# Kernel optimization log

Measured on AMD Instinct MI355X. Metric: run time of the kernel, lower is better.

The kernel has to match this reference:

```python
import jax, jax.numpy as jnp
import numpy as np

NUM_VARIABLES = 20
NUM_LAYERS = 3
NUM_CONSTRAINTS = 64
NUM_STATES = 2 ** NUM_VARIABLES
TOP_K = 10  # min(10, num_states)


def _state_bits():
    # bits[i, v] = v-th bit of i, MSB first (matches format(i, '0{n}b'))
    idx = jnp.arange(NUM_STATES, dtype=jnp.int32)
    shifts = jnp.arange(NUM_VARIABLES - 1, -1, -1, dtype=jnp.int32)
    return ((idx[:, None] >> shifts[None, :]) & 1).astype(jnp.float32)


def setup_inputs() -> dict:
    key = jax.random.key(0)
    k1, k2, k3 = jax.random.split(key, 3)
    return {
        "problem_constraints": jax.random.normal(k1, (NUM_CONSTRAINTS, NUM_VARIABLES), dtype=jnp.float32),
        "beta_params": jax.random.normal(k2, (NUM_LAYERS,), dtype=jnp.float32) * 0.1,
        "gamma_params": jax.random.normal(k3, (NUM_LAYERS,), dtype=jnp.float32) * 0.1,
    }


def reference(problem_constraints, beta_params, gamma_params):
    bits = _state_bits()  # [S, n]
    # cost_function evaluated on every basis state (vectorized over 2^n states)
    viol = bits @ problem_constraints.T  # [S, C]
    costs = jnp.sum(jnp.maximum(viol - 1.0, 0.0) ** 2, axis=1) + 0.1 * jnp.sum(bits, axis=1)
    costs = jax.lax.stop_gradient(costs)  # torch fills costs via .item(), detaching them

    amps = jnp.full((NUM_STATES,), 1.0 / np.sqrt(NUM_STATES), dtype=jnp.float32)
    for layer in range(NUM_LAYERS):
        # problem unitary: exp(-i*gamma*cost) applied to real amps, then cast back
        # to float32 (torch .to(float) keeps the real part) => multiply by cos.
        amps = amps * jnp.cos(gamma_params[layer] * costs)
        # mixer: mixed[i] = amps[i] + 0.1*sin(beta) * sum_bit amps[i ^ (1<<bit)]
        grid = amps.reshape((2,) * NUM_VARIABLES)
        nb = jnp.zeros_like(grid)
        for ax in range(NUM_VARIABLES):  # structural loop over qubit axes
            nb = nb + jnp.flip(grid, axis=ax)
        mixed = amps + 0.1 * jnp.sin(beta_params[layer]) * nb.reshape(-1)
        amps = mixed / jnp.linalg.norm(mixed)

    probs = amps ** 2  # |amplitude|^2 (amps are real after the casts)
    _, top_idx = jax.lax.top_k(probs, TOP_K)
    top_assignments = bits[top_idx]  # [K, n]
    assignment_costs = costs[top_idx]  # same formula as cost_function on each
    best = jnp.argmin(assignment_costs)
    optimal_assignment = top_assignments[best]
    optimal_cost = assignment_costs[best]
    return (optimal_assignment, optimal_cost, probs, top_assignments, assignment_costs)
```

## Files before the change

kernel.cpp:

```cpp
#include <hip/hip_runtime.h>
#include <math.h>

#define NV 20
#define NC 64
#define NSTATES (1u << 20)
#define TOPK 10
#define NB1 256
#define NCAND (NB1 * TOPK)

__global__ __launch_bounds__(256) void k_costs(const float* __restrict__ C,
                                               float* __restrict__ costs,
                                               float* __restrict__ ph0,
                                               const float* __restrict__ gamma,
                                               double* __restrict__ scal,
                                               unsigned* __restrict__ ctr) {
    __shared__ float CT[NV][NC];
    __shared__ float lowT[8][NC];
    const int tid = threadIdx.x;

    if (blockIdx.x == 0) {
        if (tid < 8) scal[tid] = 0.0;
        if (tid == 8) *ctr = 0u;
    }

    for (int e = tid; e < NC * NV; e += 256) {
        int c = e / NV, j = e % NV;
        CT[j][c] = C[e];
    }
    for (int e = tid; e < 8 * NC; e += 256) {
        int m = e >> 6, c = e & 63;
        float v = 0.0f;
        if (m & 1) v += C[c * NV + 19];
        if (m & 2) v += C[c * NV + 18];
        if (m & 4) v += C[c * NV + 17];
        lowT[m][c] = v;
    }
    __syncthreads();

    unsigned t = blockIdx.x * 256u + (unsigned)tid;
    float g0 = gamma[0];

    float4 b[16];
    #pragma unroll
    for (int q = 0; q < 16; ++q) b[q] = make_float4(-1.f, -1.f, -1.f, -1.f);
    #pragma unroll
    for (int k = 0; k < 17; ++k) {
        float bf = (float)((t >> k) & 1u);
        const float4* row = (const float4*)(&CT[16 - k][0]);
        #pragma unroll
        for (int q = 0; q < 16; ++q) {
            float4 cv = row[q];
            b[q].x = fmaf(bf, cv.x, b[q].x);
            b[q].y = fmaf(bf, cv.y, b[q].y);
            b[q].z = fmaf(bf, cv.z, b[q].z);
            b[q].w = fmaf(bf, cv.w, b[q].w);
        }
    }

    float res[8], ph[8];
    #pragma unroll
    for (int s = 0; s < 8; ++s) {
        unsigned i = t * 8u + (unsigned)s;
        float cost = 0.1f * (float)__popc(i);
        const float4* lrow = (const float4*)(&lowT[s][0]);
        #pragma unroll
        for (int q = 0; q < 16; ++q) {
            float4 lv = lrow[q];
            float4 v;
            v.x = b[q].x + lv.x; v.y = b[q].y + lv.y;
            v.z = b[q].z + lv.z; v.w = b[q].w + lv.w;
            float r;
            r = fmaxf(v.x, 0.f); cost = fmaf(r, r, cost);
            r = fmaxf(v.y, 0.f); cost = fmaf(r, r, cost);
            r = fmaxf(v.z, 0.f); cost = fmaf(r, r, cost);
            r = fmaxf(v.w, 0.f); cost = fmaf(r, r, cost);
        }
        res[s] = cost;
        ph[s] = 0x1p-10f * cosf(g0 * cost);
    }
    float4* co = (float4*)(costs + (size_t)t * 8u);
    co[0] = make_float4(res[0], res[1], res[2], res[3]);
    co[1] = make_float4(res[4], res[5], res[6], res[7]);
    float4* po = (float4*)(ph0 + (size_t)t * 8u);
    po[0] = make_float4(ph[0], ph[1], ph[2], ph[3]);
    po[1] = make_float4(ph[4], ph[5], ph[6], ph[7]);
}

template <int LAYER, bool ALIN, bool ALOUT>
__global__ __launch_bounds__(1024, 4) void k_mix(const float* __restrict__ pin,
                                                 const float* __restrict__ costs,
                                                 float* __restrict__ pout,
                                                 const float* __restrict__ gamma,
                                                 const float* __restrict__ beta,
                                                 double* __restrict__ scal) {
    __shared__ float4 tile[1024];
    __shared__ double dpart[16];
    const unsigned lq = threadIdx.x;
    const unsigned i4 = blockIdx.x * 1024u + lq;
    float s = 0.1f * sinf(beta[LAYER]);
    float prevscale = (LAYER == 0) ? 1.0f : (float)(1.0 / sqrt(scal[LAYER - 1]));

    auto ld4 = [&](unsigned j4) -> float4 {
        if (ALIN) return ((const float4*)pin)[j4];
        float4 a;
        a.x = pin[4u * j4 + 0]; a.y = pin[4u * j4 + 1];
        a.z = pin[4u * j4 + 2]; a.w = pin[4u * j4 + 3];
        return a;
    };

    float4 own = ld4(i4);
    tile[lq] = own;

    float4 gv[8];
    #pragma unroll
    for (int p = 19; p >= 12; --p) gv[19 - p] = ld4(i4 ^ (1u << (p - 2)));

    __syncthreads();

    float4 nb = make_float4(0.f, 0.f, 0.f, 0.f);
    #pragma unroll
    for (int u = 0; u < 8; ++u) {
        nb.x += gv[u].x; nb.y += gv[u].y; nb.z += gv[u].z; nb.w += gv[u].w;
    }
    #pragma unroll
    for (int p = 11; p >= 2; --p) {
        float4 v = tile[lq ^ (1u << (p - 2))];
        nb.x += v.x; nb.y += v.y; nb.z += v.z; nb.w += v.w;
    }
    nb.x += own.z; nb.y += own.w; nb.z += own.x; nb.w += own.y;
    nb.x += own.y; nb.y += own.x; nb.z += own.w; nb.w += own.z;

    float4 m;
    m.x = prevscale * fmaf(s, nb.x, own.x);
    m.y = prevscale * fmaf(s, nb.y, own.y);
    m.z = prevscale * fmaf(s, nb.z, own.z);
    m.w = prevscale * fmaf(s, nb.w, own.w);

    float4 o;
    if (LAYER < 2) {
        float gn = gamma[LAYER + 1];
        float4 c = ((const float4*)costs)[i4];
        o.x = m.x * cosf(gn * c.x);
        o.y = m.y * cosf(gn * c.y);
        o.z = m.z * cosf(gn * c.z);
        o.w = m.w * cosf(gn * c.w);
    } else {
        o = m;
    }
    if (ALOUT) {
        ((float4*)pout)[i4] = o;
    } else {
        pout[4u * i4 + 0] = o.x; pout[4u * i4 + 1] = o.y;
        pout[4u * i4 + 2] = o.z; pout[4u * i4 + 3] = o.w;
    }

    double ss = (double)m.x * m.x + (double)m.y * m.y +
                (double)m.z * m.z + (double)m.w * m.w;
    #pragma unroll
    for (int off = 32; off > 0; off >>= 1) ss += __shfl_down(ss, off);
    int wid = threadIdx.x >> 6;
    if ((threadIdx.x & 63) == 0) dpart[wid] = ss;
    __syncthreads();
    if (threadIdx.x == 0) {
        double t = 0.0;
        #pragma unroll
        for (int w = 0; w < 16; ++w) t += dpart[w];
        atomicAdd(&scal[LAYER], t);
    }
}

template <bool ALIN>
__global__ __launch_bounds__(256) void k_ptop(const float* __restrict__ A,
                                              const double* __restrict__ scal2,
                                              const float* __restrict__ costs,
                                              float* __restrict__ out,
                                              unsigned long long* __restrict__ cand,
                                              unsigned* __restrict__ ctr) {
    __shared__ unsigned long long warr[4];
    __shared__ int lastblk;
    __shared__ unsigned topi[TOPK];
    __shared__ float topc[TOPK];
    const int tid = threadIdx.x;
    float* probs_out = out + 21;
    unsigned b4 = blockIdx.x * 1024u;
    float scale = (float)(1.0 / sqrt(*scal2));

    unsigned long long k[16];
    #pragma unroll
    for (int u = 0; u < 4; ++u) {
        unsigned j4 = b4 + (unsigned)tid + 256u * u;
        float4 v;
        if (ALIN) v = ((const float4*)A)[j4];
        else {
            v.x = A[4u * j4 + 0]; v.y = A[4u * j4 + 1];
            v.z = A[4u * j4 + 2]; v.w = A[4u * j4 + 3];
        }
        float4 p;
        p.x = v.x * scale; p.x *= p.x;
        p.y = v.y * scale; p.y *= p.y;
        p.z = v.z * scale; p.z *= p.z;
        p.w = v.w * scale; p.w *= p.w;
        unsigned e0 = 4u * j4;
        probs_out[e0 + 0] = p.x; probs_out[e0 + 1] = p.y;
        probs_out[e0 + 2] = p.z; probs_out[e0 + 3] = p.w;
        k[4 * u + 0] = ((unsigned long long)__float_as_uint(p.x) << 32) | (unsigned long long)(0xFFFFFFFFu - (e0 + 0));
        k[4 * u + 1] = ((unsigned long long)__float_as_uint(p.y) << 32) | (unsigned long long)(0xFFFFFFFFu - (e0 + 1));
        k[4 * u + 2] = ((unsigned long long)__float_as_uint(p.z) << 32) | (unsigned long long)(0xFFFFFFFFu - (e0 + 2));
        k[4 * u + 3] = ((unsigned long long)__float_as_uint(p.w) << 32) | (unsigned long long)(0xFFFFFFFFu - (e0 + 3));
    }

    for (int r = 0; r < TOPK; ++r) {
        unsigned long long loc = 0ull;
        #pragma unroll
        for (int j = 0; j < 16; ++j) if (k[j] > loc) loc = k[j];
        #pragma unroll
        for (int off = 32; off > 0; off >>= 1) {
            unsigned long long o = __shfl_down(loc, off);
            if (o > loc) loc = o;
        }
        if ((tid & 63) == 0) warr[tid >> 6] = loc;
        __syncthreads();
        unsigned long long win = warr[0];
        if (warr[1] > win) win = warr[1];
        if (warr[2] > win) win = warr[2];
        if (warr[3] > win) win = warr[3];
        __syncthreads();
        #pragma unroll
        for (int j = 0; j < 16; ++j) if (k[j] == win) k[j] = 0ull;
        if (tid == 0) cand[blockIdx.x * TOPK + r] = win;
    }

    __threadfence();
    if (tid == 0) {
        unsigned old = atomicAdd(ctr, 1u);
        lastblk = (old == NB1 - 1) ? 1 : 0;
    }
    __syncthreads();
    if (!lastblk) return;
    __threadfence();

    unsigned long long c2[TOPK];
    #pragma unroll
    for (int u = 0; u < TOPK; ++u) c2[u] = cand[tid + 256 * u];

    for (int r = 0; r < TOPK; ++r) {
        unsigned long long loc = 0ull;
        #pragma unroll
        for (int u = 0; u < TOPK; ++u) if (c2[u] > loc) loc = c2[u];
        #pragma unroll
        for (int off = 32; off > 0; off >>= 1) {
            unsigned long long o = __shfl_down(loc, off);
            if (o > loc) loc = o;
        }
        if ((tid & 63) == 0) warr[tid >> 6] = loc;
        __syncthreads();
        unsigned long long win = warr[0];
        if (warr[1] > win) win = warr[1];
        if (warr[2] > win) win = warr[2];
        if (warr[3] > win) win = warr[3];
        __syncthreads();
        #pragma unroll
        for (int u = 0; u < TOPK; ++u) if (c2[u] == win) c2[u] = 0ull;
        if (tid == 0) topi[r] = 0xFFFFFFFFu - (unsigned)(win & 0xFFFFFFFFull);
        __syncthreads();
    }

    const unsigned S = NSTATES;
    if (tid < TOPK * NV) {
        int kk = tid / NV, vv = tid % NV;
        out[21 + S + (unsigned)tid] = (float)((topi[kk] >> (NV - 1 - vv)) & 1u);
    }
    if (tid < TOPK) {
        float c = costs[topi[tid]];
        topc[tid] = c;
        out[21 + S + TOPK * NV + (unsigned)tid] = c;
    }
    __syncthreads();
    if (tid == 0) {
        int best = 0;
        for (int kk = 1; kk < TOPK; ++kk)
            if (topc[kk] < topc[best]) best = kk;
        unsigned gi = topi[best];
        for (int vv = 0; vv < NV; ++vv)
            out[vv] = (float)((gi >> (NV - 1 - vv)) & 1u);
        out[NV] = topc[best];
    }
}

extern "C" void kernel_launch(void* const* d_in, const int* in_sizes, int n_in,
                              void* d_out_, int out_size, void* d_ws, size_t ws_size,
                              hipStream_t stream) {
    (void)in_sizes; (void)n_in; (void)out_size;
    const float* C     = (const float*)d_in[0];
    const float* beta  = (const float*)d_in[1];
    const float* gamma = (const float*)d_in[2];
    float* out = (float*)d_out_;
    char* ws = (char*)d_ws;
    const size_t S4 = (size_t)NSTATES * sizeof(float);

    double* scal = (double*)ws;
    unsigned* ctr = (unsigned*)(ws + 64);
    unsigned long long* cand = (unsigned long long*)(ws + 1024);
    float* costs = (float*)(ws + 32768);
    float* A     = (float*)(ws + 32768 + S4);
    const size_t need_full = 32768 + 3 * S4;
    bool wsbig = (ws_size >= need_full);
    float* B = wsbig ? (float*)(ws + 32768 + 2 * S4) : (out + 21);

    k_costs<<<512, 256, 0, stream>>>(C, costs, A, gamma, scal, ctr);

    if (wsbig) {
        k_mix<0, true, true ><<<256, 1024, 0, stream>>>(A, costs, B, gamma, beta, scal);
        k_mix<1, true, true ><<<256, 1024, 0, stream>>>(B, costs, A, gamma, beta, scal);
        k_mix<2, true, true ><<<256, 1024, 0, stream>>>(A, costs, B, gamma, beta, scal);
        k_ptop<true ><<<NB1, 256, 0, stream>>>(B, scal + 2, costs, out, cand, ctr);
    } else {
        k_mix<0, true, false><<<256, 1024, 0, stream>>>(A, costs, B, gamma, beta, scal);
        k_mix<1, false, true><<<256, 1024, 0, stream>>>(B, costs, A, gamma, beta, scal);
        k_mix<2, true, false><<<256, 1024, 0, stream>>>(A, costs, B, gamma, beta, scal);
        k_ptop<false><<<NB1, 256, 0, stream>>>(B, scal + 2, costs, out, cand, ctr);
    }
}
```

Before: 89.55 us.

## Fuse cost, mixer layers and top-k into one cooperative persistent kernel

```diff
diff --git a/kernel.cpp b/kernel.cpp
--- a/kernel.cpp
+++ b/kernel.cpp
@@ -1,12 +1,284 @@
 #include <hip/hip_runtime.h>
+#include <hip/hip_cooperative_groups.h>
 #include <math.h>
+
+namespace cg = cooperative_groups;
 
 #define NV 20
 #define NC 64
 #define NSTATES (1u << 20)
 #define TOPK 10
-#define NB1 256
-#define NCAND (NB1 * TOPK)
+#define NBLK 256
+#define NTHR 1024
+#define NCAND (NBLK * TOPK)
+#define NB1F 256
+
+template <bool ALB>
+__global__ __launch_bounds__(NTHR, 4) void k_all(
+    const float* __restrict__ C,
+    const float* __restrict__ beta,
+    const float* __restrict__ gamma,
+    float* __restrict__ costs,
+    float* __restrict__ A,
+    float* __restrict__ B,
+    float* __restrict__ out,
+    double* __restrict__ scal,
+    unsigned long long* __restrict__ cand) {
+
+  cg::grid_group grid = cg::this_grid();
+
+  __shared__ float4 tile[NTHR];
+  __shared__ float CT[17][NC];
+  __shared__ float lowT[8][NC];
+  __shared__ double dpart[16];
+  __shared__ unsigned long long warr[16];
+  __shared__ unsigned long long winS;
+  __shared__ unsigned topi[TOPK];
+  __shared__ float topc[TOPK];
+
+  const int tid = threadIdx.x;
+  const unsigned t = blockIdx.x * (unsigned)NTHR + (unsigned)tid;
+
+  if (blockIdx.x == 0 && tid < 8) scal[tid] = 0.0;
+
+  for (int e = tid; e < 17 * NC; e += NTHR) {
+    int k = e / NC, c = e % NC;
+    CT[k][c] = C[c * NV + (16 - k)];
+  }
+  for (int e = tid; e < 8 * NC; e += NTHR) {
+    int m = e >> 6, c = e & 63;
+    float v = 0.0f;
+    if (m & 1) v += C[c * NV + 19];
+    if (m & 2) v += C[c * NV + 18];
+    if (m & 4) v += C[c * NV + 17];
+    lowT[m][c] = v;
+  }
+  __syncthreads();
+
+  float4 b[16];
+  #pragma unroll
+  for (int q = 0; q < 16; ++q) b[q] = make_float4(-1.f, -1.f, -1.f, -1.f);
+  #pragma unroll
+  for (int k = 0; k < 17; ++k) {
+    float bf = (float)((t >> (k + 1)) & 1u);
+    const float4* row = (const float4*)(&CT[k][0]);
+    #pragma unroll
+    for (int q = 0; q < 16; ++q) {
+      float4 cv = row[q];
+      b[q].x = fmaf(bf, cv.x, b[q].x);
+      b[q].y = fmaf(bf, cv.y, b[q].y);
+      b[q].z = fmaf(bf, cv.z, b[q].z);
+      b[q].w = fmaf(bf, cv.w, b[q].w);
+    }
+  }
+
+  float g0 = gamma[0];
+  float c_own[4], p_arr[4];
+  #pragma unroll
+  for (int s = 0; s < 4; ++s) {
+    unsigned i = 4u * t + (unsigned)s;
+    float cost = 0.1f * (float)__popc(i);
+    int m = (int)(((t & 1u) << 2) | (unsigned)s);
+    const float4* lrow = (const float4*)(&lowT[m][0]);
+    #pragma unroll
+    for (int q = 0; q < 16; ++q) {
+      float4 lv = lrow[q];
+      float4 v;
+      v.x = b[q].x + lv.x; v.y = b[q].y + lv.y;
+      v.z = b[q].z + lv.z; v.w = b[q].w + lv.w;
+      float r;
+      r = fmaxf(v.x, 0.f); cost = fmaf(r, r, cost);
+      r = fmaxf(v.y, 0.f); cost = fmaf(r, r, cost);
+      r = fmaxf(v.z, 0.f); cost = fmaf(r, r, cost);
+      r = fmaxf(v.w, 0.f); cost = fmaf(r, r, cost);
+    }
+    c_own[s] = cost;
+    p_arr[s] = 0x1p-10f * cosf(g0 * cost);
+  }
+  ((float4*)costs)[t] = make_float4(c_own[0], c_own[1], c_own[2], c_own[3]);
+  float4 pin_own = make_float4(p_arr[0], p_arr[1], p_arr[2], p_arr[3]);
+  ((float4*)A)[t] = pin_own;
+
+  grid.sync();
+
+  float4 m2_own = make_float4(0.f, 0.f, 0.f, 0.f);
+  #pragma unroll
+  for (int L = 0; L < 3; ++L) {
+    const float* pin = (L == 1) ? B : A;
+    const bool pinAligned = (L == 1) ? ALB : true;
+    float s = 0.1f * sinf(beta[L]);
+    float prevscale = (L == 0) ? 1.0f : (float)(1.0 / sqrt(scal[L - 1]));
+
+    tile[tid] = pin_own;
+    float4 gv[8];
+    #pragma unroll
+    for (int p = 19; p >= 12; --p) {
+      unsigned j4 = t ^ (1u << (p - 2));
+      if (pinAligned) gv[19 - p] = ((const float4*)pin)[j4];
+      else {
+        gv[19 - p].x = pin[4u * j4 + 0]; gv[19 - p].y = pin[4u * j4 + 1];
+        gv[19 - p].z = pin[4u * j4 + 2]; gv[19 - p].w = pin[4u * j4 + 3];
+      }
+    }
+    __syncthreads();
+
+    float4 nb = make_float4(0.f, 0.f, 0.f, 0.f);
+    #pragma unroll
+    for (int u = 0; u < 8; ++u) {
+      nb.x += gv[u].x; nb.y += gv[u].y; nb.z += gv[u].z; nb.w += gv[u].w;
+    }
+    #pragma unroll
+    for (int p = 11; p >= 2; --p) {
+      float4 v = tile[tid ^ (1 << (p - 2))];
+      nb.x += v.x; nb.y += v.y; nb.z += v.z; nb.w += v.w;
+    }
+    nb.x += pin_own.z; nb.y += pin_own.w; nb.z += pin_own.x; nb.w += pin_own.y;
+    nb.x += pin_own.y; nb.y += pin_own.x; nb.z += pin_own.w; nb.w += pin_own.z;
+
+    float4 m;
+    m.x = prevscale * fmaf(s, nb.x, pin_own.x);
+    m.y = prevscale * fmaf(s, nb.y, pin_own.y);
+    m.z = prevscale * fmaf(s, nb.z, pin_own.z);
+    m.w = prevscale * fmaf(s, nb.w, pin_own.w);
+
+    double ss = (double)m.x * m.x + (double)m.y * m.y +
+                (double)m.z * m.z + (double)m.w * m.w;
+    #pragma unroll
+    for (int off = 32; off > 0; off >>= 1) ss += __shfl_down(ss, off);
+    if ((tid & 63) == 0) dpart[tid >> 6] = ss;
+    __syncthreads();
+    if (tid == 0) {
+      double tt = 0.0;
+      #pragma unroll
+      for (int w = 0; w < 16; ++w) tt += dpart[w];
+      atomicAdd(&scal[L], tt);
+    }
+
+    if (L < 2) {
+      float gn = gamma[L + 1];
+      float4 o;
+      o.x = m.x * cosf(gn * c_own[0]);
+      o.y = m.y * cosf(gn * c_own[1]);
+      o.z = m.z * cosf(gn * c_own[2]);
+      o.w = m.w * cosf(gn * c_own[3]);
+      if (L == 0) {
+        if (ALB) ((float4*)B)[t] = o;
+        else {
+          B[4u * t + 0] = o.x; B[4u * t + 1] = o.y;
+          B[4u * t + 2] = o.z; B[4u * t + 3] = o.w;
+        }
+      } else {
+        ((float4*)A)[t] = o;
+      }
+      pin_own = o;
+    } else {
+      m2_own = m;
+    }
+    grid.sync();
+  }
+
+  float scale2 = (float)(1.0 / sqrt(scal[2]));
+  float4 pr;
+  pr.x = m2_own.x * scale2; pr.x *= pr.x;
+  pr.y = m2_own.y * scale2; pr.y *= pr.y;
+  pr.z = m2_own.z * scale2; pr.z *= pr.z;
+  pr.w = m2_own.w * scale2; pr.w *= pr.w;
+  float* probs = out + 21;
+  unsigned e0 = 4u * t;
+  probs[e0 + 0] = pr.x; probs[e0 + 1] = pr.y;
+  probs[e0 + 2] = pr.z; probs[e0 + 3] = pr.w;
+
+  unsigned long long k[4];
+  k[0] = ((unsigned long long)__float_as_uint(pr.x) << 32) | (unsigned long long)(0xFFFFFFFFu - (e0 + 0));
+  k[1] = ((unsigned long long)__float_as_uint(pr.y) << 32) | (unsigned long long)(0xFFFFFFFFu - (e0 + 1));
+  k[2] = ((unsigned long long)__float_as_uint(pr.z) << 32) | (unsigned long long)(0xFFFFFFFFu - (e0 + 2));
+  k[3] = ((unsigned long long)__float_as_uint(pr.w) << 32) | (unsigned long long)(0xFFFFFFFFu - (e0 + 3));
+
+  for (int r = 0; r < TOPK; ++r) {
+    unsigned long long loc = k[0];
+    if (k[1] > loc) loc = k[1];
+    if (k[2] > loc) loc = k[2];
+    if (k[3] > loc) loc = k[3];
+    #pragma unroll
+    for (int off = 32; off > 0; off >>= 1) {
+      unsigned long long o = __shfl_down(loc, off);
+      if (o > loc) loc = o;
+    }
+    if ((tid & 63) == 0) warr[tid >> 6] = loc;
+    __syncthreads();
+    if (tid == 0) {
+      unsigned long long win = warr[0];
+      #pragma unroll
+      for (int w = 1; w < 16; ++w) if (warr[w] > win) win = warr[w];
+      winS = win;
+      cand[blockIdx.x * TOPK + r] = win;
+    }
+    __syncthreads();
+    unsigned long long win = winS;
+    if (k[0] == win) k[0] = 0ull;
+    if (k[1] == win) k[1] = 0ull;
+    if (k[2] == win) k[2] = 0ull;
+    if (k[3] == win) k[3] = 0ull;
+    __syncthreads();
+  }
+
+  grid.sync();
+
+  if (blockIdx.x != 0) return;
+
+  unsigned long long c2[3] = {0ull, 0ull, 0ull};
+  #pragma unroll
+  for (int u = 0; u < 3; ++u) {
+    int j = tid + NTHR * u;
+    if (j < NCAND) c2[u] = cand[j];
+  }
+  for (int r = 0; r < TOPK; ++r) {
+    unsigned long long loc = c2[0];
+    if (c2[1] > loc) loc = c2[1];
+    if (c2[2] > loc) loc = c2[2];
+    #pragma unroll
+    for (int off = 32; off > 0; off >>= 1) {
+      unsigned long long o = __shfl_down(loc, off);
+      if (o > loc) loc = o;
+    }
+    if ((tid & 63) == 0) warr[tid >> 6] = loc;
+    __syncthreads();
+    if (tid == 0) {
+      unsigned long long win = warr[0];
+      #pragma unroll
+      for (int w = 1; w < 16; ++w) if (warr[w] > win) win = warr[w];
+      winS = win;
+      topi[r] = 0xFFFFFFFFu - (unsigned)(win & 0xFFFFFFFFull);
+    }
+    __syncthreads();
+    unsigned long long win = winS;
+    if (c2[0] == win) c2[0] = 0ull;
+    if (c2[1] == win) c2[1] = 0ull;
+    if (c2[2] == win) c2[2] = 0ull;
+    __syncthreads();
+  }
+
+  const unsigned S = NSTATES;
+  if (tid < TOPK * NV) {
+    int kk = tid / NV, vv = tid % NV;
+    out[21 + S + (unsigned)tid] = (float)((topi[kk] >> (NV - 1 - vv)) & 1u);
+  }
+  if (tid < TOPK) {
+    float c = costs[topi[tid]];
+    topc[tid] = c;
+    out[21 + S + TOPK * NV + (unsigned)tid] = c;
+  }
+  __syncthreads();
+  if (tid == 0) {
+    int best = 0;
+    for (int kk = 1; kk < TOPK; ++kk)
+      if (topc[kk] < topc[best]) best = kk;
+    unsigned gi = topi[best];
+    for (int vv = 0; vv < NV; ++vv)
+      out[vv] = (float)((gi >> (NV - 1 - vv)) & 1u);
+    out[NV] = topc[best];
+  }
+}
 
 __global__ __launch_bounds__(256) void k_costs(const float* __restrict__ C,
                                                float* __restrict__ costs,
@@ -17,16 +289,11 @@
     __shared__ float CT[NV][NC];
     __shared__ float lowT[8][NC];
     const int tid = threadIdx.x;
-
     if (blockIdx.x == 0) {
         if (tid < 8) scal[tid] = 0.0;
         if (tid == 8) *ctr = 0u;
     }
-
-    for (int e = tid; e < NC * NV; e += 256) {
-        int c = e / NV, j = e % NV;
-        CT[j][c] = C[e];
-    }
+    for (int e = tid; e < NC * NV; e += 256) { int c = e / NV, j = e % NV; CT[j][c] = C[e]; }
     for (int e = tid; e < 8 * NC; e += 256) {
         int m = e >> 6, c = e & 63;
         float v = 0.0f;
@@ -36,10 +303,8 @@
         lowT[m][c] = v;
     }
     __syncthreads();
-
     unsigned t = blockIdx.x * 256u + (unsigned)tid;
     float g0 = gamma[0];
-
     float4 b[16];
     #pragma unroll
     for (int q = 0; q < 16; ++q) b[q] = make_float4(-1.f, -1.f, -1.f, -1.f);
@@ -56,7 +321,6 @@
             b[q].w = fmaf(bf, cv.w, b[q].w);
         }
     }
-
     float res[8], ph[8];
     #pragma unroll
     for (int s = 0; s < 8; ++s) {
@@ -99,7 +363,6 @@
     const unsigned i4 = blockIdx.x * 1024u + lq;
     float s = 0.1f * sinf(beta[LAYER]);
     float prevscale = (LAYER == 0) ? 1.0f : (float)(1.0 / sqrt(scal[LAYER - 1]));
-
     auto ld4 = [&](unsigned j4) -> float4 {
         if (ALIN) return ((const float4*)pin)[j4];
         float4 a;
@@ -107,21 +370,15 @@
         a.z = pin[4u * j4 + 2]; a.w = pin[4u * j4 + 3];
         return a;
     };
-
     float4 own = ld4(i4);
     tile[lq] = own;
-
     float4 gv[8];
     #pragma unroll
     for (int p = 19; p >= 12; --p) gv[19 - p] = ld4(i4 ^ (1u << (p - 2)));
-
-    __syncthreads();
-
+    __syncthreads();
     float4 nb = make_float4(0.f, 0.f, 0.f, 0.f);
     #pragma unroll
-    for (int u = 0; u < 8; ++u) {
-        nb.x += gv[u].x; nb.y += gv[u].y; nb.z += gv[u].z; nb.w += gv[u].w;
-    }
+    for (int u = 0; u < 8; ++u) { nb.x += gv[u].x; nb.y += gv[u].y; nb.z += gv[u].z; nb.w += gv[u].w; }
     #pragma unroll
     for (int p = 11; p >= 2; --p) {
         float4 v = tile[lq ^ (1u << (p - 2))];
@@ -129,43 +386,34 @@
     }
     nb.x += own.z; nb.y += own.w; nb.z += own.x; nb.w += own.y;
     nb.x += own.y; nb.y += own.x; nb.z += own.w; nb.w += own.z;
-
     float4 m;
     m.x = prevscale * fmaf(s, nb.x, own.x);
     m.y = prevscale * fmaf(s, nb.y, own.y);
     m.z = prevscale * fmaf(s, nb.z, own.z);
     m.w = prevscale * fmaf(s, nb.w, own.w);
-
     float4 o;
     if (LAYER < 2) {
         float gn = gamma[LAYER + 1];
         float4 c = ((const float4*)costs)[i4];
-        o.x = m.x * cosf(gn * c.x);
-        o.y = m.y * cosf(gn * c.y);
-        o.z = m.z * cosf(gn * c.z);
-        o.w = m.w * cosf(gn * c.w);
-    } else {
-        o = m;
-    }
-    if (ALOUT) {
-        ((float4*)pout)[i4] = o;
-    } else {
+        o.x = m.x * cosf(gn * c.x); o.y = m.y * cosf(gn * c.y);
+        o.z = m.z * cosf(gn * c.z); o.w = m.w * cosf(gn * c.w);
+    } else o = m;
+    if (ALOUT) ((float4*)pout)[i4] = o;
+    else {
         pout[4u * i4 + 0] = o.x; pout[4u * i4 + 1] = o.y;
         pout[4u * i4 + 2] = o.z; pout[4u * i4 + 3] = o.w;
     }
-
-    double ss = (double)m.x * m.x + (double)m.y * m.y +
-                (double)m.z * m.z + (double)m.w * m.w;
+    double ss = (double)m.x * m.x + (double)m.y * m.y + (double)m.z * m.z + (double)m.w * m.w;
     #pragma unroll
     for (int off = 32; off > 0; off >>= 1) ss += __shfl_down(ss, off);
     int wid = threadIdx.x >> 6;
     if ((threadIdx.x & 63) == 0) dpart[wid] = ss;
     __syncthreads();
     if (threadIdx.x == 0) {
-        double t = 0.0;
-        #pragma unroll
-        for (int w = 0; w < 16; ++w) t += dpart[w];
-        atomicAdd(&scal[LAYER], t);
+        double tt = 0.0;
+        #pragma unroll
+        for (int w = 0; w < 16; ++w) tt += dpart[w];
+        atomicAdd(&scal[LAYER], tt);
     }
 }
 
@@ -184,7 +432,6 @@
     float* probs_out = out + 21;
     unsigned b4 = blockIdx.x * 1024u;
     float scale = (float)(1.0 / sqrt(*scal2));
-
     unsigned long long k[16];
     #pragma unroll
     for (int u = 0; u < 4; ++u) {
@@ -208,7 +455,6 @@
         k[4 * u + 2] = ((unsigned long long)__float_as_uint(p.z) << 32) | (unsigned long long)(0xFFFFFFFFu - (e0 + 2));
         k[4 * u + 3] = ((unsigned long long)__float_as_uint(p.w) << 32) | (unsigned long long)(0xFFFFFFFFu - (e0 + 3));
     }
-
     for (int r = 0; r < TOPK; ++r) {
         unsigned long long loc = 0ull;
         #pragma unroll
@@ -229,20 +475,17 @@
         for (int j = 0; j < 16; ++j) if (k[j] == win) k[j] = 0ull;
         if (tid == 0) cand[blockIdx.x * TOPK + r] = win;
     }
-
     __threadfence();
     if (tid == 0) {
         unsigned old = atomicAdd(ctr, 1u);
-        lastblk = (old == NB1 - 1) ? 1 : 0;
+        lastblk = (old == NB1F - 1) ? 1 : 0;
     }
     __syncthreads();
     if (!lastblk) return;
     __threadfence();
-
     unsigned long long c2[TOPK];
     #pragma unroll
     for (int u = 0; u < TOPK; ++u) c2[u] = cand[tid + 256 * u];
-
     for (int r = 0; r < TOPK; ++r) {
         unsigned long long loc = 0ull;
         #pragma unroll
@@ -264,7 +507,6 @@
         if (tid == 0) topi[r] = 0xFFFFFFFFu - (unsigned)(win & 0xFFFFFFFFull);
         __syncthreads();
     }
-
     const unsigned S = NSTATES;
     if (tid < TOPK * NV) {
         int kk = tid / NV, vv = tid % NV;
@@ -307,17 +549,25 @@
     bool wsbig = (ws_size >= need_full);
     float* B = wsbig ? (float*)(ws + 32768 + 2 * S4) : (out + 21);
 
+    hipError_t err;
+    {
+        void* args[] = {(void*)&C, (void*)&beta, (void*)&gamma, (void*)&costs,
+                        (void*)&A, (void*)&B, (void*)&out, (void*)&scal, (void*)&cand};
+        const void* fn = wsbig ? (const void*)k_all<true> : (const void*)k_all<false>;
+        err = hipLaunchCooperativeKernel(fn, dim3(NBLK), dim3(NTHR), args, 0, stream);
+    }
+    if (err == hipSuccess) return;
+
     k_costs<<<512, 256, 0, stream>>>(C, costs, A, gamma, scal, ctr);
-
     if (wsbig) {
         k_mix<0, true, true ><<<256, 1024, 0, stream>>>(A, costs, B, gamma, beta, scal);
         k_mix<1, true, true ><<<256, 1024, 0, stream>>>(B, costs, A, gamma, beta, scal);
         k_mix<2, true, true ><<<256, 1024, 0, stream>>>(A, costs, B, gamma, beta, scal);
-        k_ptop<true ><<<NB1, 256, 0, stream>>>(B, scal + 2, costs, out, cand, ctr);
+        k_ptop<true ><<<NB1F, 256, 0, stream>>>(B, scal + 2, costs, out, cand, ctr);
     } else {
         k_mix<0, true, false><<<256, 1024, 0, stream>>>(A, costs, B, gamma, beta, scal);
         k_mix<1, false, true><<<256, 1024, 0, stream>>>(B, costs, A, gamma, beta, scal);
         k_mix<2, true, false><<<256, 1024, 0, stream>>>(A, costs, B, gamma, beta, scal);
-        k_ptop<false><<<NB1, 256, 0, stream>>>(B, scal + 2, costs, out, cand, ctr);
+        k_ptop<false><<<NB1F, 256, 0, stream>>>(B, scal + 2, costs, out, cand, ctr);
     }
 }
```

Result: slower. 218.9 us (+144.4%).
